# Kernel tuning notes

Measured on AMD Instinct MI355X. Metric: run time of the kernel, lower is better.

The kernel has to match this reference:

```python
import jax, jax.numpy as jnp
import numpy as np

L, H, D, HS, DFF, V, B, T = 4, 16, 1024, 64, 5120, 32000, 2, 1024
EPS = 1e-5


def setup_inputs() -> dict:
    key = jax.random.key(0)
    ks = iter(jax.random.split(key, 40))
    def nrm(shape):
        return jax.random.normal(next(ks), shape, dtype=jnp.float32) * 0.02
    inp = {}
    inp['idx'] = jax.random.randint(next(ks), (B, T), 0, V)
    inp['tok_emb'] = nrm((V, D))
    inp['pos_emb'] = nrm((T, D))
    for s in ('u', 'm'):  # u = unmasked heads, m = masked (causal) heads
        inp['Wq_' + s] = nrm((L, H, D, HS)); inp['bq_' + s] = jnp.zeros((L, H, HS), jnp.float32)
        inp['Wk_' + s] = nrm((L, H, D, HS)); inp['bk_' + s] = jnp.zeros((L, H, HS), jnp.float32)
        inp['Wv_' + s] = nrm((L, H, D, HS)); inp['bv_' + s] = jnp.zeros((L, H, HS), jnp.float32)
        inp['Wp_' + s] = nrm((L, D, D));     inp['bp_' + s] = jnp.zeros((L, D), jnp.float32)
    inp['W1'] = nrm((L, D, DFF)); inp['b1'] = jnp.zeros((L, DFF), jnp.float32)
    inp['W2'] = nrm((L, DFF, D)); inp['b2'] = jnp.zeros((L, D), jnp.float32)
    ones = jnp.ones((L, D), jnp.float32); zer = jnp.zeros((L, D), jnp.float32)
    inp['lnf_g'] = ones; inp['lnf_b'] = zer     # LayerNorm inside FeedForward
    inp['n1_g'] = ones;  inp['n1_b'] = zer      # Block.norm1
    inp['n2_g'] = ones;  inp['n2_b'] = zer      # Block.norm2
    inp['nf_g'] = jnp.ones((D,), jnp.float32); inp['nf_b'] = jnp.zeros((D,), jnp.float32)
    inp['Wfin'] = nrm((D, V)); inp['bfin'] = jnp.zeros((V,), jnp.float32)
    return inp


def _ln(x, g, b):
    mu = jnp.mean(x, -1, keepdims=True)
    var = jnp.mean((x - mu) ** 2, -1, keepdims=True)
    return (x - mu) / jnp.sqrt(var + EPS) * g + b


def _attn(xn, Wq, bq, Wk, bk, Wv, bv, Wp, bp, causal):
    # xn: [B,T,D]; Wq/Wk/Wv: [H,D,HS] (all heads batched in one einsum)
    q = jnp.einsum('btd,hde->bhte', xn, Wq) + bq[:, None, :]
    k = jnp.einsum('btd,hde->bhte', xn, Wk) + bk[:, None, :]
    v = jnp.einsum('btd,hde->bhte', xn, Wv) + bv[:, None, :]
    w = jnp.einsum('bhte,bhse->bhts', q, k) * (HS ** -0.5)
    if causal:
        mask = jnp.tril(jnp.ones((w.shape[-2], w.shape[-1]), bool))
        w = jnp.where(mask, w, -jnp.inf)
    w = jax.nn.softmax(w, axis=-1)
    o = jnp.einsum('bhts,bhse->bhte', w, v)
    o = o.transpose(0, 2, 1, 3).reshape(xn.shape[0], xn.shape[1], -1)  # concat heads
    return o @ Wp + bp


def _ffn(x, W1, b1, W2, b2, g, b):
    h = jax.nn.leaky_relu(x @ W1 + b1, negative_slope=0.01)
    return _ln(h @ W2 + b2, g, b)


def reference(idx, tok_emb, pos_emb,
              Wq_u, bq_u, Wk_u, bk_u, Wv_u, bv_u, Wp_u, bp_u,
              Wq_m, bq_m, Wk_m, bk_m, Wv_m, bv_m, Wp_m, bp_m,
              W1, b1, W2, b2, lnf_g, lnf_b, n1_g, n1_b, n2_g, n2_b,
              nf_g, nf_b, Wfin, bfin):
    Tn = idx.shape[1]
    x = tok_emb[idx] + pos_emb[:Tn]
    for l in range(L):
        # exact quirky Block wiring from the original code
        x2 = x + _attn(_ln(x, n1_g[l], n1_b[l]), Wq_u[l], bq_u[l], Wk_u[l], bk_u[l],
                       Wv_u[l], bv_u[l], Wp_u[l], bp_u[l], False)
        x = x2 + _ln(_ffn(_ln(x2, n2_g[l], n2_b[l]), W1[l], b1[l], W2[l], b2[l],
                          lnf_g[l], lnf_b[l]), n1_g[l], n1_b[l])
        x2 = x + _attn(_ln(x, n1_g[l], n1_b[l]), Wq_m[l], bq_m[l], Wk_m[l], bk_m[l],
                       Wv_m[l], bv_m[l], Wp_m[l], bp_m[l], True)
        x = x2 + _ln(_ffn(_ln(x2, n2_g[l], n2_b[l]), W1[l], b1[l], W2[l], b2[l],
                          lnf_g[l], lnf_b[l]), n2_g[l], n2_b[l])
    x = _ln(x, nf_g, nf_b)
    return x @ Wfin + bfin  # logits [B,T,V]; targets=None path -> loss is None
```

## Files before the change

kernel.cpp:

```cpp
#include <hip/hip_runtime.h>
#include <hip/hip_bf16.h>
#include <math.h>

#define LNUM 4
#define H 16
#define D 1024
#define HS 64
#define DFF 5120
#define V 32000
#define BB 2
#define T 1024
#define M (BB*T)
#define EPS 1e-5f

typedef __attribute__((ext_vector_type(8))) short bf16x8;
typedef __attribute__((ext_vector_type(4))) float f32x4;

__device__ __forceinline__ void gload16(const void* g, void* l) {
    __builtin_amdgcn_global_load_lds(
        (const __attribute__((address_space(1))) void*)g,
        (__attribute__((address_space(3))) void*)l, 16, 0, 0);
}

__device__ __forceinline__ float wred_sum(float v) {
    #pragma unroll
    for (int off = 32; off; off >>= 1) v += __shfl_xor(v, off, 64);
    return v;
}

__global__ __launch_bounds__(256) void embed_kernel(const int* __restrict__ idx,
        const float* __restrict__ tok, const float* __restrict__ pos,
        float* __restrict__ x) {
    int row = blockIdx.x;
    int t = row & (T - 1);
    int tok_id = idx[row];
    int c = threadIdx.x * 4;
    float4 a = *(const float4*)&tok[(size_t)tok_id * D + c];
    float4 p = *(const float4*)&pos[(size_t)t * D + c];
    a.x += p.x; a.y += p.y; a.z += p.z; a.w += p.w;
    *(float4*)&x[(size_t)row * D + c] = a;
}

__global__ __launch_bounds__(256) void ln_bf16_w4_kernel(const float* __restrict__ in,
        const float* __restrict__ g, const float* __restrict__ b,
        __hip_bfloat16* __restrict__ out) {
    int w = threadIdx.x >> 6, lane = threadIdx.x & 63;
    int row = blockIdx.x * 4 + w;
    const float* rp = in + (size_t)row * D;
    float4 xv[4];
    float s = 0.f;
    #pragma unroll
    for (int c = 0; c < 4; ++c) {
        xv[c] = *(const float4*)&rp[c * 256 + lane * 4];
        s += xv[c].x + xv[c].y + xv[c].z + xv[c].w;
    }
    float mu = wred_sum(s) * (1.0f / D);
    float vs = 0.f;
    #pragma unroll
    for (int c = 0; c < 4; ++c) {
        xv[c].x -= mu; xv[c].y -= mu; xv[c].z -= mu; xv[c].w -= mu;
        vs += xv[c].x*xv[c].x + xv[c].y*xv[c].y + xv[c].z*xv[c].z + xv[c].w*xv[c].w;
    }
    float rs = rsqrtf(wred_sum(vs) * (1.0f / D) + EPS);
    #pragma unroll
    for (int c = 0; c < 4; ++c) {
        int j = c * 256 + lane * 4;
        float4 gv = *(const float4*)&g[j];
        float4 bv = *(const float4*)&b[j];
        union { ushort4 u4; __hip_bfloat16 h[4]; } pk;
        pk.h[0] = __float2bfloat16(xv[c].x * rs * gv.x + bv.x);
        pk.h[1] = __float2bfloat16(xv[c].y * rs * gv.y + bv.y);
        pk.h[2] = __float2bfloat16(xv[c].z * rs * gv.z + bv.z);
        pk.h[3] = __float2bfloat16(xv[c].w * rs * gv.w + bv.w);
        *(ushort4*)&out[(size_t)row * D + j] = pk.u4;
    }
}

template<int NP>
__global__ __launch_bounds__(256) void ffn_tail_kernel(
        const float* __restrict__ part, const float* __restrict__ b2,
        const float* __restrict__ g1, const float* __restrict__ b1,
        const float* __restrict__ g2, const float* __restrict__ b2g,
        const float* __restrict__ res, float* __restrict__ xout,
        const float* __restrict__ gn, const float* __restrict__ bn,
        __hip_bfloat16* __restrict__ xnout) {
    const size_t MD = (size_t)M * D;
    int w = threadIdx.x >> 6, lane = threadIdx.x & 63;
    int row = blockIdx.x * 4 + w;
    size_t ro = (size_t)row * D;
    float4 f[4];
    float s = 0.f;
    #pragma unroll
    for (int c = 0; c < 4; ++c) {
        int j = c * 256 + lane * 4;
        float4 acc = *(const float4*)&b2[j];
        #pragma unroll
        for (int pI = 0; pI < NP; ++pI) {
            float4 pv = *(const float4*)&part[pI * MD + ro + j];
            acc.x += pv.x; acc.y += pv.y; acc.z += pv.z; acc.w += pv.w;
        }
        f[c] = acc;
        s += acc.x + acc.y + acc.z + acc.w;
    }
    float mu = wred_sum(s) * (1.0f / D);
    float vs = 0.f;
    #pragma unroll
    for (int c = 0; c < 4; ++c) {
        f[c].x -= mu; f[c].y -= mu; f[c].z -= mu; f[c].w -= mu;
        vs += f[c].x*f[c].x + f[c].y*f[c].y + f[c].z*f[c].z + f[c].w*f[c].w;
    }
    float rs = rsqrtf(wred_sum(vs) * (1.0f / D) + EPS);
    float s2 = 0.f;
    #pragma unroll
    for (int c = 0; c < 4; ++c) {
        int j = c * 256 + lane * 4;
        float4 gv = *(const float4*)&g1[j];
        float4 bv = *(const float4*)&b1[j];
        f[c].x = f[c].x * rs * gv.x + bv.x;
        f[c].y = f[c].y * rs * gv.y + bv.y;
        f[c].z = f[c].z * rs * gv.z + bv.z;
        f[c].w = f[c].w * rs * gv.w + bv.w;
        s2 += f[c].x + f[c].y + f[c].z + f[c].w;
    }
    float mu2 = wred_sum(s2) * (1.0f / D);
    float vs2 = 0.f;
    #pragma unroll
    for (int c = 0; c < 4; ++c) {
        f[c].x -= mu2; f[c].y -= mu2; f[c].z -= mu2; f[c].w -= mu2;
        vs2 += f[c].x*f[c].x + f[c].y*f[c].y + f[c].z*f[c].z + f[c].w*f[c].w;
    }
    float rs2 = rsqrtf(wred_sum(vs2) * (1.0f / D) + EPS);
    float s3 = 0.f;
    #pragma unroll
    for (int c = 0; c < 4; ++c) {
        int j = c * 256 + lane * 4;
        float4 gv = *(const float4*)&g2[j];
        float4 bv = *(const float4*)&b2g[j];
        float4 rv = *(const float4*)&res[ro + j];
        f[c].x = rv.x + f[c].x * rs2 * gv.x + bv.x;
        f[c].y = rv.y + f[c].y * rs2 * gv.y + bv.y;
        f[c].z = rv.z + f[c].z * rs2 * gv.z + bv.z;
        f[c].w = rv.w + f[c].w * rs2 * gv.w + bv.w;
        *(float4*)&xout[ro + j] = f[c];
        s3 += f[c].x + f[c].y + f[c].z + f[c].w;
    }
    float mu3 = wred_sum(s3) * (1.0f / D);
    float vs3 = 0.f;
    #pragma unroll
    for (int c = 0; c < 4; ++c) {
        f[c].x -= mu3; f[c].y -= mu3; f[c].z -= mu3; f[c].w -= mu3;
        vs3 += f[c].x*f[c].x + f[c].y*f[c].y + f[c].z*f[c].z + f[c].w*f[c].w;
    }
    float rs3 = rsqrtf(wred_sum(vs3) * (1.0f / D) + EPS);
    #pragma unroll
    for (int c = 0; c < 4; ++c) {
        int j = c * 256 + lane * 4;
        float4 gv = *(const float4*)&gn[j];
        float4 bv = *(const float4*)&bn[j];
        union { ushort4 u4; __hip_bfloat16 h[4]; } pk;
        pk.h[0] = __float2bfloat16(f[c].x * rs3 * gv.x + bv.x);
        pk.h[1] = __float2bfloat16(f[c].y * rs3 * gv.y + bv.y);
        pk.h[2] = __float2bfloat16(f[c].z * rs3 * gv.z + bv.z);
        pk.h[3] = __float2bfloat16(f[c].w * rs3 * gv.w + bv.w);
        *(ushort4*)&xnout[ro + j] = pk.u4;
    }
}

__global__ __launch_bounds__(256) void transpose_bf16_kernel(
        const float* __restrict__ in, __hip_bfloat16* __restrict__ out,
        int R, int C, size_t zin, size_t zout) {
    __shared__ float t[32][33];
    in += (size_t)blockIdx.z * zin; out += (size_t)blockIdx.z * zout;
    int tx = threadIdx.x & 31, ty = threadIdx.x >> 5;
    int c0 = blockIdx.x * 32, r0 = blockIdx.y * 32;
    #pragma unroll
    for (int i = 0; i < 4; ++i)
        t[ty + i * 8][tx] = in[(size_t)(r0 + ty + i * 8) * C + c0 + tx];
    __syncthreads();
    #pragma unroll
    for (int i = 0; i < 4; ++i)
        out[(size_t)(c0 + ty + i * 8) * R + r0 + tx] = __float2bfloat16(t[tx][ty + i * 8]);
}

__global__ __launch_bounds__(256) void transpose_qkv_kernel(
        const float* __restrict__ Wq, const float* __restrict__ Wk,
        const float* __restrict__ Wv, short* __restrict__ outT) {
    __shared__ float t[32][33];
    int z = blockIdx.z;
    int which = z >> 4, h = z & 15;
    const float* in = (which == 0 ? Wq : which == 1 ? Wk : Wv) + (size_t)h * D * HS;
    __hip_bfloat16* out = (__hip_bfloat16*)outT + ((size_t)which * H + h) * HS * D;
    int tx = threadIdx.x & 31, ty = threadIdx.x >> 5;
    int c0 = blockIdx.x * 32, r0 = blockIdx.y * 32;
    #pragma unroll
    for (int i = 0; i < 4; ++i)
        t[ty + i * 8][tx] = in[(size_t)(r0 + ty + i * 8) * HS + c0 + tx];
    __syncthreads();
    #pragma unroll
    for (int i = 0; i < 4; ++i)
        out[(size_t)(c0 + ty + i * 8) * D + r0 + tx] = __float2bfloat16(t[tx][ty + i * 8]);
}

__global__ __launch_bounds__(256) void transpose_v_kernel(const short* __restrict__ in,
        short* __restrict__ out) {
    __shared__ short t[32][33];
    int z = blockIdx.z;
    in  += (size_t)z * T * HS;
    out += (size_t)z * HS * T;
    int tx = threadIdx.x & 31, ty = threadIdx.x >> 5;
    int c0 = blockIdx.x * 32, r0 = blockIdx.y * 32;
    #pragma unroll
    for (int i = 0; i < 4; ++i)
        t[ty + i * 8][tx] = in[(size_t)(r0 + ty + i * 8) * HS + c0 + tx];
    __syncthreads();
    #pragma unroll
    for (int i = 0; i < 4; ++i)
        out[(size_t)(c0 + ty + i * 8) * T + r0 + tx] = t[tx][ty + i * 8];
}

template<int EPI>
__global__ __launch_bounds__(512, 2) void mm256_kernel(
        const short* __restrict__ A, const short* __restrict__ BT,
        const float* __restrict__ bias0, float* __restrict__ C0,
        __hip_bfloat16* __restrict__ Cbf, int N, int Kloop, int lda) {
    __shared__ __align__(16) char LA[2][2][256 * 64];
    __shared__ __align__(16) char LB[2][2][256 * 64];
    int tid = threadIdx.x;
    int lane = tid & 63, wid = tid >> 6;
    int wr = wid >> 2, wc = wid & 3;
    int l15 = lane & 15, l16 = lane >> 4;

    int nwg = gridDim.x;
    int bid = blockIdx.x;
    int q = nwg >> 3, r = nwg & 7;
    int xcd = bid & 7, loc = bid >> 3;
    int wg = (xcd < r ? xcd * (q + 1) : r * (q + 1) + (xcd - r) * q) + loc;
    int m0 = (wg & 7) * 256;
    int n0 = (wg >> 3) * 256;

    const size_t lda2 = (size_t)lda * 2;
    const char* Agc = (const char*)A + (size_t)m0 * lda2;
    const char* Bgc = (const char*)BT + (size_t)n0 * lda2;

    f32x4 acc[8][4] = {};
    bf16x8 af[8], bfr[2];

    auto stA = [&](int buf, int kh, int kt) {
        #pragma unroll
        for (int i = 0; i < 2; ++i) {
            int o = i * 8192 + tid * 16;
            int row = o >> 6, col = o & 63;
            gload16(Agc + (size_t)row * lda2 + kt * 128 + kh * 64 +
                    (col ^ (((row >> 1) & 3) << 4)), LA[buf][kh] + o);
        }
    };
    auto stB = [&](int buf, int kh, int kt) {
        #pragma unroll
        for (int i = 0; i < 2; ++i) {
            int o = i * 8192 + tid * 16;
            int row = o >> 6, col = o & 63;
            gload16(Bgc + (size_t)row * lda2 + kt * 128 + kh * 64 +
                    (col ^ (((row >> 1) & 3) << 4)), LB[buf][kh] + o);
        }
    };
    auto rdA = [&](int buf, int kk) {
        #pragma unroll
        for (int mf = 0; mf < 8; ++mf) {
            int row = wr * 128 + mf * 16 + l15;
            af[mf] = *(const bf16x8*)(LA[buf][kk] + row * 64 +
                      ((l16 * 16) ^ (((row >> 1) & 3) << 4)));
        }
    };
    auto rdB = [&](int buf, int kk, int nh) {
        #pragma unroll
        for (int nf = 0; nf < 2; ++nf) {
            int row = wc * 64 + nh * 32 + nf * 16 + l15;
            bfr[nf] = *(const bf16x8*)(LB[buf][kk] + row * 64 +
                       ((l16 * 16) ^ (((row >> 1) & 3) << 4)));
        }
    };
    auto mfma16 = [&](int nh) {
        __builtin_amdgcn_s_setprio(1);
        #pragma unroll
        for (int mf = 0; mf < 8; ++mf) {
            acc[mf][nh * 2 + 0] = __builtin_amdgcn_mfma_f32_16x16x32_bf16(
                af[mf], bfr[0], acc[mf][nh * 2 + 0], 0, 0, 0);
            acc[mf][nh * 2 + 1] = __builtin_amdgcn_mfma_f32_16x16x32_bf16(
                af[mf], bfr[1], acc[mf][nh * 2 + 1], 0, 0, 0);
        }
        __builtin_amdgcn_s_setprio(0);
        __builtin_amdgcn_s_barrier();
    };

    const int NT = Kloop / 64;
    stA(0, 0, 0); stB(0, 0, 0); stA(0, 1, 0); stB(0, 1, 0);
    stA(1, 0, 1); stB(1, 0, 1);

    for (int t = 0; t < NT; ++t) {
        int buf = t & 1;
        if (t + 1 < NT) { asm volatile("s_waitcnt vmcnt(4)" ::: "memory"); }
        else            { asm volatile("s_waitcnt vmcnt(0)" ::: "memory"); }
        __builtin_amdgcn_sched_barrier(0);
        __builtin_amdgcn_s_barrier();
        __builtin_amdgcn_sched_barrier(0);
        rdA(buf, 0); rdB(buf, 0, 0);
        if (t + 1 < NT) stA(buf ^ 1, 1, t + 1);
        __builtin_amdgcn_s_barrier();
        asm volatile("s_waitcnt lgkmcnt(0)" ::: "memory");
        __builtin_amdgcn_sched_barrier(0);
        mfma16(0);
        rdB(buf, 0, 1);
        if (t + 1 < NT) stB(buf ^ 1, 1, t + 1);
        __builtin_amdgcn_s_barrier();
        asm volatile("s_waitcnt lgkmcnt(0)" ::: "memory");
        __builtin_amdgcn_sched_barrier(0);
        mfma16(1);
        rdA(buf, 1); rdB(buf, 1, 0);
        if (t + 2 < NT) stA(buf, 0, t + 2);
        __builtin_amdgcn_s_barrier();
        asm volatile("s_waitcnt lgkmcnt(0)" ::: "memory");
        __builtin_amdgcn_sched_barrier(0);
        mfma16(0);
        rdB(buf, 1, 1);
        if (t + 2 < NT) stB(buf, 0, t + 2);
        __builtin_amdgcn_s_barrier();
        asm volatile("s_waitcnt lgkmcnt(0)" ::: "memory");
        __builtin_amdgcn_sched_barrier(0);
        mfma16(1);
    }

    #pragma unroll
    for (int mf = 0; mf < 8; ++mf) {
        #pragma unroll
        for (int nf = 0; nf < 4; ++nf) {
            int col = n0 + wc * 64 + nf * 16 + l15;
            float bv = bias0[col];
            #pragma unroll
            for (int rr = 0; rr < 4; ++rr) {
                int row = m0 + wr * 128 + mf * 16 + l16 * 4 + rr;
                float v = acc[mf][nf][rr] + bv;
                if (EPI == 0) {
                    C0[(size_t)row * N + col] = v;
                } else {
                    v = v > 0.f ? v : 0.01f * v;
                    Cbf[(size_t)row * N + col] = __float2bfloat16(v);
                }
            }
        }
    }
}

template<int BM, int EPI>
__global__ __launch_bounds__(256) void mm_bf16_kernel(
        const short* __restrict__ A, const short* __restrict__ BT,
        const float* __restrict__ bias0, const float* __restrict__ bias1,
        const float* __restrict__ bias2, const float* __restrict__ res,
        float* __restrict__ C0, float* __restrict__ C1, float* __restrict__ C2,
        __hip_bfloat16* __restrict__ Cbf, int N, int Kloop, int lda) {
    constexpr int MI = BM / 32;
    __shared__ __align__(16) char As[2][BM * 128];
    __shared__ __align__(16) char Bs[2][128 * 128];
    int nwg = gridDim.x * gridDim.y;
    int bid = blockIdx.y * gridDim.x + blockIdx.x;
    int bx = blockIdx.x, by = blockIdx.y;
    if (!(nwg & 7)) {
        int s = (bid & 7) * (nwg >> 3) + (bid >> 3);
        bx = s % gridDim.x; by = s / gridDim.x;
    }
    int tid = threadIdx.x;
    int lane = tid & 63, wid = tid >> 6;
    int wr = wid >> 1, wc = wid & 1;
    int l15 = lane & 15, l16 = lane >> 4;
    int m0 = bx * BM, n0 = by * 128;
    f32x4 acc[MI][4] = {};

    const size_t lda2 = (size_t)lda * 2;
    const char* Agc = (const char*)A + (size_t)m0 * lda2 + (size_t)blockIdx.z * Kloop * 2;
    const char* Bgc = (const char*)BT + (size_t)n0 * lda2 + (size_t)blockIdx.z * Kloop * 2;

    auto stage = [&](int buf, int kbyte) {
        #pragma unroll
        for (int i = 0; i < BM / 32; ++i) {
            int o = i * 4096 + tid * 16;
            int row = o >> 7, col = o & 127;
            gload16(Agc + (size_t)row * lda2 + kbyte + (col ^ ((row & 7) << 4)),
                    As[buf] + o);
        }
        #pragma unroll
        for (int i = 0; i < 4; ++i) {
            int o = i * 4096 + tid * 16;
            int row = o >> 7, col = o & 127;
            gload16(Bgc + (size_t)row * lda2 + kbyte + (col ^ ((row & 7) << 4)),
                    Bs[buf] + o);
        }
    };
    auto compute = [&](int buf) {
        #pragma unroll
        for (int kk = 0; kk < 2; ++kk) {
            bf16x8 af[MI], bfr[4];
            #pragma unroll
            for (int mi = 0; mi < MI; ++mi) {
                int row = wr * (BM / 2) + mi * 16 + l15;
                af[mi] = *(const bf16x8*)(As[buf] + row * 128 +
                          ((kk * 64 + l16 * 16) ^ ((row & 7) << 4)));
            }
            #pragma unroll
            for (int ni = 0; ni < 4; ++ni) {
                int row = wc * 64 + ni * 16 + l15;
                bfr[ni] = *(const bf16x8*)(Bs[buf] + row * 128 +
                          ((kk * 64 + l16 * 16) ^ ((row & 7) << 4)));
            }
            __builtin_amdgcn_s_setprio(1);
            #pragma unroll
            for (int mi = 0; mi < MI; ++mi)
                #pragma unroll
                for (int ni = 0; ni < 4; ++ni)
                    acc[mi][ni] = __builtin_amdgcn_mfma_f32_16x16x32_bf16(
                        af[mi], bfr[ni], acc[mi][ni], 0, 0, 0);
            __builtin_amdgcn_s_setprio(0);
        }
    };

    const int NT = Kloop / 64;
    stage(0, 0);
    stage(1, 128);
    for (int t = 0; t < NT; ++t) {
        if (t < NT - 1) {
            if constexpr (BM == 128) asm volatile("s_waitcnt vmcnt(8)" ::: "memory");
            else                     asm volatile("s_waitcnt vmcnt(6)" ::: "memory");
        } else {
            asm volatile("s_waitcnt vmcnt(0)" ::: "memory");
        }
        __builtin_amdgcn_sched_barrier(0);
        __builtin_amdgcn_s_barrier();
        __builtin_amdgcn_sched_barrier(0);
        compute(t & 1);
        __builtin_amdgcn_s_barrier();
        __builtin_amdgcn_sched_barrier(0);
        if (t + 2 < NT) stage(t & 1, (t + 2) * 128);
    }

    int rbase = m0 + wr * (BM / 2) + l16 * 4;
    int cbase = n0 + wc * 64 + l15;
    size_t zoff = (EPI == 4) ? (size_t)blockIdx.z * M * N : 0;
    #pragma unroll
    for (int mi = 0; mi < MI; ++mi) {
        #pragma unroll
        for (int ni = 0; ni < 4; ++ni) {
            int col = cbase + ni * 16;
            float bv = 0.f;
            if (EPI == 3) {
                int z = col >> 10, nn = col & 1023;
                bv = (z == 0 ? bias0 : z == 1 ? bias1 : bias2)[nn];
            } else if (EPI != 4) bv = bias0[col];
            #pragma unroll
            for (int r = 0; r < 4; ++r) {
                int row = rbase + mi * 16 + r;
                float v = acc[mi][ni][r] + bv;
                if (EPI == 0) {
                    C0[(size_t)row * N + col] = v;
                } else if (EPI == 1) {
                    C0[(size_t)row * N + col] = v + res[(size_t)row * N + col];
                } else if (EPI == 2) {
                    v = v > 0.f ? v : 0.01f * v;
                    Cbf[(size_t)row * N + col] = __float2bfloat16(v);
                } else if (EPI == 4) {
                    C0[zoff + (size_t)row * N + col] = v;
                } else {
                    int z = col >> 10;
                    int hh = (col >> 6) & 15, e = col & 63;
                    int b = row >> 10, t2 = row & (T - 1);
                    __hip_bfloat16* dst = (__hip_bfloat16*)(z == 0 ? C0 : (z == 1 ? C1 : C2));
                    dst[(((size_t)(b * H + hh)) * T + t2) * HS + e] = __float2bfloat16(v);
                }
            }
        }
    }
}

template<int CAUSAL>
__global__ __launch_bounds__(256) void attn_mfma_kernel(
        const short* __restrict__ q, const short* __restrict__ k,
        const short* __restrict__ vt, __hip_bfloat16* __restrict__ att) {
    __shared__ __align__(16) short Ks[128 * 64];
    __shared__ __align__(16) short Vs[64 * 128];
    __shared__ __align__(16) short Ps[4][16 * 128];
    int bh = blockIdx.y;
    int bI = bh >> 4, h = bh & 15;
    int tix = blockIdx.x;
    if (CAUSAL) tix = (tix & 1) ? (15 - (tix >> 1)) : (tix >> 1);
    int t0 = tix * 64;
    int tid = threadIdx.x;
    int lane = tid & 63, w = tid >> 6;
    int l15 = lane & 15, l16 = lane >> 4;

    const short* Qg = q + ((size_t)bh * T + t0 + w * 16 + l15) * HS + l16 * 8;
    bf16x8 qf0 = *(const bf16x8*)Qg;
    bf16x8 qf1 = *(const bf16x8*)(Qg + 32);

    const char* Kg = (const char*)(k + (size_t)bh * T * HS);
    const char* Vg = (const char*)(vt + (size_t)bh * HS * T);

    float m_run[4] = {-1e30f, -1e30f, -1e30f, -1e30f};
    float l_run[4] = {0.f, 0.f, 0.f, 0.f};
    f32x4 acc_o[4] = {};
    char* Pw = (char*)Ps[w];
    int pswz = l15 << 4;

    int n_tiles = CAUSAL ? (t0 / 128 + 1) : (T / 128);
    for (int it = 0; it < n_tiles; ++it) {
        int s0 = it * 128;
        __syncthreads();
        #pragma unroll
        for (int i = 0; i < 4; ++i) {
            int o = i * 4096 + tid * 16;
            int row = o >> 7, bir = o & 127;
            gload16(Kg + (size_t)(s0 + row) * 128 + (bir ^ ((row & 7) << 4)),
                    (char*)Ks + o);
        }
        #pragma unroll
        for (int i = 0; i < 4; ++i) {
            int o = i * 4096 + tid * 16;
            int row = o >> 8, bb = o & 255;
            gload16(Vg + (size_t)row * 2048 + s0 * 2 + (bb ^ ((row & 15) << 4)),
                    (char*)Vs + o);
        }
        __syncthreads();

        f32x4 acc_s[8] = {};
        __builtin_amdgcn_s_setprio(1);
        #pragma unroll
        for (int c = 0; c < 8; ++c) {
            int row = c * 16 + l15;
            const char* kb_ = (const char*)Ks + row * 128;
            int swz = (row & 7) << 4;
            bf16x8 kf0 = *(const bf16x8*)(kb_ + ((l16 * 16) ^ swz));
            bf16x8 kf1 = *(const bf16x8*)(kb_ + ((64 + l16 * 16) ^ swz));
            acc_s[c] = __builtin_amdgcn_mfma_f32_16x16x32_bf16(qf0, kf0, acc_s[c], 0, 0, 0);
            acc_s[c] = __builtin_amdgcn_mfma_f32_16x16x32_bf16(qf1, kf1, acc_s[c], 0, 0, 0);
        }
        __builtin_amdgcn_s_setprio(0);

        bool domask = CAUSAL && (it == n_tiles - 1);
        #pragma unroll
        for (int r = 0; r < 4; ++r) {
            float sc[8];
            #pragma unroll
            for (int c = 0; c < 8; ++c) {
                float s = acc_s[c][r];
                if (domask && (s0 + c * 16 + l15) > (t0 + w * 16 + l16 * 4 + r)) s = -1e30f;
                sc[c] = s;
            }
            float tm = fmaxf(fmaxf(fmaxf(sc[0], sc[1]), fmaxf(sc[2], sc[3])),
                             fmaxf(fmaxf(sc[4], sc[5]), fmaxf(sc[6], sc[7])));
            tm = fmaxf(tm, __shfl_xor(tm, 1, 16));
            tm = fmaxf(tm, __shfl_xor(tm, 2, 16));
            tm = fmaxf(tm, __shfl_xor(tm, 4, 16));
            tm = fmaxf(tm, __shfl_xor(tm, 8, 16));
            float mn = fmaxf(m_run[r], tm);
            int prow = l16 * 4 + r;
            int pswzr = prow << 4;
            float ls = 0.f;
            #pragma unroll
            for (int c = 0; c < 8; ++c) {
                float pv = __expf(0.125f * (sc[c] - mn));
                int pbyte = prow * 256 + (((c * 16 + l15) * 2) ^ pswzr);
                *(__hip_bfloat16*)(Pw + pbyte) = __float2bfloat16(pv);
                ls += pv;
            }
            ls += __shfl_xor(ls, 1, 16);
            ls += __shfl_xor(ls, 2, 16);
            ls += __shfl_xor(ls, 4, 16);
            ls += __shfl_xor(ls, 8, 16);
            float alpha = __expf(0.125f * (m_run[r] - mn));
            l_run[r] = l_run[r] * alpha + ls;
            m_run[r] = mn;
            acc_o[0][r] *= alpha; acc_o[1][r] *= alpha;
            acc_o[2][r] *= alpha; acc_o[3][r] *= alpha;
        }

        const char* Pb = Pw + l15 * 256;
        bf16x8 pa[4];
        #pragma unroll
        for (int t = 0; t < 4; ++t)
            pa[t] = *(const bf16x8*)(Pb + ((t * 64 + l16 * 16) ^ pswz));
        __builtin_amdgcn_s_setprio(1);
        #pragma unroll
        for (int ni = 0; ni < 4; ++ni) {
            int row = ni * 16 + l15;
            const char* vb_ = (const char*)Vs + row * 256;
            int swz = (row & 15) << 4;
            #pragma unroll
            for (int t = 0; t < 4; ++t) {
                bf16x8 vf = *(const bf16x8*)(vb_ + ((t * 64 + l16 * 16) ^ swz));
                acc_o[ni] = __builtin_amdgcn_mfma_f32_16x16x32_bf16(pa[t], vf, acc_o[ni], 0, 0, 0);
            }
        }
        __builtin_amdgcn_s_setprio(0);
    }

    float inv[4];
    #pragma unroll
    for (int r = 0; r < 4; ++r) inv[r] = 1.0f / l_run[r];
    #pragma unroll
    for (int ni = 0; ni < 4; ++ni) {
        #pragma unroll
        for (int r = 0; r < 4; ++r) {
            size_t orow = ((size_t)(bI * T) + t0 + w * 16 + l16 * 4 + r) * D
                        + h * HS + ni * 16 + l15;
            att[orow] = __float2bfloat16(acc_o[ni][r] * inv[r]);
        }
    }
}

extern "C" void kernel_launch(void* const* d_in, const int* in_sizes, int n_in,
                              void* d_out, int out_size, void* d_ws, size_t ws_size,
                              hipStream_t stream) {
    const int*   idx     = (const int*)d_in[0];
    const float* tok_emb = (const float*)d_in[1];
    const float* pos_emb = (const float*)d_in[2];
    const float* Wq_u = (const float*)d_in[3],  *bq_u = (const float*)d_in[4];
    const float* Wk_u = (const float*)d_in[5],  *bk_u = (const float*)d_in[6];
    const float* Wv_u = (const float*)d_in[7],  *bv_u = (const float*)d_in[8];
    const float* Wp_u = (const float*)d_in[9],  *bp_u = (const float*)d_in[10];
    const float* Wq_m = (const float*)d_in[11], *bq_m = (const float*)d_in[12];
    const float* Wk_m = (const float*)d_in[13], *bk_m = (const float*)d_in[14];
    const float* Wv_m = (const float*)d_in[15], *bv_m = (const float*)d_in[16];
    const float* Wp_m = (const float*)d_in[17], *bp_m = (const float*)d_in[18];
    const float* W1   = (const float*)d_in[19], *b1   = (const float*)d_in[20];
    const float* W2   = (const float*)d_in[21], *b2   = (const float*)d_in[22];
    const float* lnf_g = (const float*)d_in[23], *lnf_b = (const float*)d_in[24];
    const float* n1_g  = (const float*)d_in[25], *n1_b  = (const float*)d_in[26];
    const float* n2_g  = (const float*)d_in[27], *n2_b  = (const float*)d_in[28];
    const float* nf_g  = (const float*)d_in[29], *nf_b  = (const float*)d_in[30];
    const float* Wfin  = (const float*)d_in[31], *bfin  = (const float*)d_in[32];
    float* out = (float*)d_out;

    char* p = (char*)d_ws;
    auto alloc = [&](size_t bytes) { char* r = p; p += (bytes + 255) & ~255ull; return r; };
    float* x    = (float*)alloc((size_t)M * D * 4);
    float* x2   = (float*)alloc((size_t)M * D * 4);
    float* w2p  = (float*)alloc((size_t)4 * M * D * 4);
    short* qbf  = (short*)alloc((size_t)M * D * 2);
    short* kbf  = (short*)alloc((size_t)M * D * 2);
    short* vbf  = (short*)alloc((size_t)M * D * 2);
    short* vtb  = (short*)alloc((size_t)M * D * 2);
    short* xnb  = (short*)alloc((size_t)M * D * 2);
    short* attb = (short*)alloc((size_t)M * D * 2);
    short* hb   = (short*)alloc((size_t)M * DFF * 2);
    short* WqkvT= (short*)alloc((size_t)3 * 1024 * 1024 * 2);
    short* WpT  = (short*)alloc((size_t)1024 * 1024 * 2);
    short* W1T  = (short*)alloc((size_t)D * DFF * 2);
    short* W2T  = (short*)alloc((size_t)DFF * D * 2);
    short* WfT  = (short*)alloc((size_t)D * V * 2);

    embed_kernel<<<M, 256, 0, stream>>>(idx, tok_emb, pos_emb, x);
    ln_bf16_w4_kernel<<<M / 4, 256, 0, stream>>>(x, n1_g, n1_b, (__hip_bfloat16*)xnb);
    transpose_bf16_kernel<<<dim3(V / 32, D / 32, 1), 256, 0, stream>>>(
        Wfin, (__hip_bfloat16*)WfT, D, V, 0, 0);

    for (int l = 0; l < LNUM; ++l) {
        const float *n1g = n1_g + l * D, *n1b = n1_b + l * D;
        const float *n2g = n2_g + l * D, *n2b = n2_b + l * D;
        const float *lfg = lnf_g + l * D, *lfb = lnf_b + l * D;
        const float *W1l = W1 + (size_t)l * D * DFF, *b1l = b1 + l * DFF;
        const float *W2l = W2 + (size_t)l * DFF * D, *b2l = b2 + l * D;
        transpose_bf16_kernel<<<dim3(DFF / 32, D / 32, 1), 256, 0, stream>>>(
            W1l, (__hip_bfloat16*)W1T, D, DFF, 0, 0);
        transpose_bf16_kernel<<<dim3(D / 32, DFF / 32, 1), 256, 0, stream>>>(
            W2l, (__hip_bfloat16*)W2T, DFF, D, 0, 0);
        for (int half = 0; half < 2; ++half) {
            const float *Wq_, *bq_, *Wk_, *bk_, *Wv_, *bv_, *Wp_, *bp_;
            if (half == 0) { Wq_ = Wq_u; bq_ = bq_u; Wk_ = Wk_u; bk_ = bk_u;
                             Wv_ = Wv_u; bv_ = bv_u; Wp_ = Wp_u; bp_ = bp_u; }
            else           { Wq_ = Wq_m; bq_ = bq_m; Wk_ = Wk_m; bk_ = bk_m;
                             Wv_ = Wv_m; bv_ = bv_m; Wp_ = Wp_m; bp_ = bp_m; }
            Wq_ += (size_t)l * H * D * HS;  bq_ += l * H * HS;
            Wk_ += (size_t)l * H * D * HS;  bk_ += l * H * HS;
            Wv_ += (size_t)l * H * D * HS;  bv_ += l * H * HS;
            Wp_ += (size_t)l * D * D;       bp_ += l * D;

            transpose_qkv_kernel<<<dim3(HS / 32, D / 32, 48), 256, 0, stream>>>(
                Wq_, Wk_, Wv_, WqkvT);
            transpose_bf16_kernel<<<dim3(D / 32, D / 32, 1), 256, 0, stream>>>(
                Wp_, (__hip_bfloat16*)WpT, D, D, 0, 0);

            mm_bf16_kernel<128, 3><<<dim3(M / 128, 3072 / 128), 256, 0, stream>>>(
                xnb, WqkvT, bq_, bk_, bv_, nullptr,
                (float*)qbf, (float*)kbf, (float*)vbf, nullptr, 3072, D, D);
            transpose_v_kernel<<<dim3(HS / 32, T / 32, BB * H), 256, 0, stream>>>(vbf, vtb);
            if (half == 0)
                attn_mfma_kernel<0><<<dim3(T / 64, BB * H), 256, 0, stream>>>(
                    qbf, kbf, vtb, (__hip_bfloat16*)attb);
            else
                attn_mfma_kernel<1><<<dim3(T / 64, BB * H), 256, 0, stream>>>(
                    qbf, kbf, vtb, (__hip_bfloat16*)attb);
            mm_bf16_kernel<64, 1><<<dim3(M / 64, D / 128), 256, 0, stream>>>(
                attb, WpT, bp_, nullptr, nullptr, x, x2, nullptr, nullptr, nullptr, D, D, D);
            ln_bf16_w4_kernel<<<M / 4, 256, 0, stream>>>(x2, n2g, n2b, (__hip_bfloat16*)xnb);
            mm256_kernel<2><<<(M / 256) * (DFF / 256), 512, 0, stream>>>(
                xnb, W1T, b1l, nullptr, (__hip_bfloat16*)hb, DFF, D, D);
            mm_bf16_kernel<128, 4><<<dim3(M / 128, D / 128, 4), 256, 0, stream>>>(
                hb, W2T, nullptr, nullptr, nullptr, nullptr, w2p, nullptr, nullptr,
                nullptr, D, DFF / 4, DFF);
            const float* og = half ? n2g : n1g;
            const float* ob = half ? n2b : n1b;
            const float* gn; const float* bn;
            if (half == 0)      { gn = n1g; bn = n1b; }
            else if (l < LNUM-1){ gn = n1_g + (l+1)*D; bn = n1_b + (l+1)*D; }
            else                { gn = nf_g; bn = nf_b; }
            ffn_tail_kernel<4><<<M / 4, 256, 0, stream>>>(
                w2p, b2l, lfg, lfb, og, ob, x2, x, gn, bn, (__hip_bfloat16*)xnb);
        }
    }
    mm256_kernel<0><<<(M / 256) * (V / 256), 512, 0, stream>>>(
        xnb, WfT, bfin, out, nullptr, V, D, D);
}
```

Before: 1.589 ms.

## Fuse embedding with LayerNorm, merge weight transposes, simplify mm256 pipeline

Folds the embedding add and the first LayerNorm into one kernel and merges the per-layer weight transpose launches (W1+W2, Wq/Wk/Wv+Wp) into single launches. This removes several kernel launches and one full pass over the activations. It also restructures the mm256 main loop to load all four B fragments at once and issue 32 MFMAs per half-step, with fewer barriers and no explicit LDS waits. That cuts synchronisation, but it raises register pressure and may expose more LDS latency.

```diff
diff --git a/kernel.cpp b/kernel.cpp
--- a/kernel.cpp
+++ b/kernel.cpp
@@ -28,17 +28,48 @@
     return v;
 }
 
-__global__ __launch_bounds__(256) void embed_kernel(const int* __restrict__ idx,
+__global__ __launch_bounds__(256) void embed_ln_kernel(const int* __restrict__ idx,
         const float* __restrict__ tok, const float* __restrict__ pos,
-        float* __restrict__ x) {
-    int row = blockIdx.x;
+        const float* __restrict__ g, const float* __restrict__ b,
+        float* __restrict__ x, __hip_bfloat16* __restrict__ xn) {
+    int w = threadIdx.x >> 6, lane = threadIdx.x & 63;
+    int row = blockIdx.x * 4 + w;
     int t = row & (T - 1);
     int tok_id = idx[row];
-    int c = threadIdx.x * 4;
-    float4 a = *(const float4*)&tok[(size_t)tok_id * D + c];
-    float4 p = *(const float4*)&pos[(size_t)t * D + c];
-    a.x += p.x; a.y += p.y; a.z += p.z; a.w += p.w;
-    *(float4*)&x[(size_t)row * D + c] = a;
+    const float* tp = tok + (size_t)tok_id * D;
+    const float* pp = pos + (size_t)t * D;
+    float4 xv[4];
+    float s = 0.f;
+    #pragma unroll
+    for (int c = 0; c < 4; ++c) {
+        int j = c * 256 + lane * 4;
+        float4 a = *(const float4*)&tp[j];
+        float4 p = *(const float4*)&pp[j];
+        a.x += p.x; a.y += p.y; a.z += p.z; a.w += p.w;
+        *(float4*)&x[(size_t)row * D + j] = a;
+        xv[c] = a;
+        s += a.x + a.y + a.z + a.w;
+    }
+    float mu = wred_sum(s) * (1.0f / D);
+    float vs = 0.f;
+    #pragma unroll
+    for (int c = 0; c < 4; ++c) {
+        xv[c].x -= mu; xv[c].y -= mu; xv[c].z -= mu; xv[c].w -= mu;
+        vs += xv[c].x*xv[c].x + xv[c].y*xv[c].y + xv[c].z*xv[c].z + xv[c].w*xv[c].w;
+    }
+    float rs = rsqrtf(wred_sum(vs) * (1.0f / D) + EPS);
+    #pragma unroll
+    for (int c = 0; c < 4; ++c) {
+        int j = c * 256 + lane * 4;
+        float4 gv = *(const float4*)&g[j];
+        float4 bv = *(const float4*)&b[j];
+        union { ushort4 u4; __hip_bfloat16 h[4]; } pk;
+        pk.h[0] = __float2bfloat16(xv[c].x * rs * gv.x + bv.x);
+        pk.h[1] = __float2bfloat16(xv[c].y * rs * gv.y + bv.y);
+        pk.h[2] = __float2bfloat16(xv[c].z * rs * gv.z + bv.z);
+        pk.h[3] = __float2bfloat16(xv[c].w * rs * gv.w + bv.w);
+        *(ushort4*)&xn[(size_t)row * D + j] = pk.u4;
+    }
 }
 
 __global__ __launch_bounds__(256) void ln_bf16_w4_kernel(const float* __restrict__ in,
@@ -168,9 +199,8 @@
 
 __global__ __launch_bounds__(256) void transpose_bf16_kernel(
         const float* __restrict__ in, __hip_bfloat16* __restrict__ out,
-        int R, int C, size_t zin, size_t zout) {
+        int R, int C) {
     __shared__ float t[32][33];
-    in += (size_t)blockIdx.z * zin; out += (size_t)blockIdx.z * zout;
     int tx = threadIdx.x & 31, ty = threadIdx.x >> 5;
     int c0 = blockIdx.x * 32, r0 = blockIdx.y * 32;
     #pragma unroll
@@ -182,23 +212,57 @@
         out[(size_t)(c0 + ty + i * 8) * R + r0 + tx] = __float2bfloat16(t[tx][ty + i * 8]);
 }
 
-__global__ __launch_bounds__(256) void transpose_qkv_kernel(
+__global__ __launch_bounds__(256) void trans_qkvp_kernel(
         const float* __restrict__ Wq, const float* __restrict__ Wk,
-        const float* __restrict__ Wv, short* __restrict__ outT) {
+        const float* __restrict__ Wv, const float* __restrict__ Wp,
+        short* __restrict__ qkvT, short* __restrict__ WpT) {
     __shared__ float t[32][33];
+    int tx = threadIdx.x & 31, ty = threadIdx.x >> 5;
     int z = blockIdx.z;
-    int which = z >> 4, h = z & 15;
-    const float* in = (which == 0 ? Wq : which == 1 ? Wk : Wv) + (size_t)h * D * HS;
-    __hip_bfloat16* out = (__hip_bfloat16*)outT + ((size_t)which * H + h) * HS * D;
+    const float* in;
+    __hip_bfloat16* out;
+    int inC, outC;
+    int r0 = blockIdx.y * 32, c0;
+    if (z < 3) {
+        int c0g = blockIdx.x * 32;
+        int h = c0g >> 6;
+        c0 = c0g & 63;
+        in = (z == 0 ? Wq : z == 1 ? Wk : Wv) + (size_t)h * D * HS;
+        out = (__hip_bfloat16*)qkvT + ((size_t)z * H + h) * HS * D;
+        inC = HS; outC = D;
+    } else {
+        c0 = blockIdx.x * 32;
+        in = Wp; out = (__hip_bfloat16*)WpT;
+        inC = D; outC = D;
+    }
+    #pragma unroll
+    for (int i = 0; i < 4; ++i)
+        t[ty + i * 8][tx] = in[(size_t)(r0 + ty + i * 8) * inC + c0 + tx];
+    __syncthreads();
+    #pragma unroll
+    for (int i = 0; i < 4; ++i)
+        out[(size_t)(c0 + ty + i * 8) * outC + r0 + tx] = __float2bfloat16(t[tx][ty + i * 8]);
+}
+
+__global__ __launch_bounds__(256) void trans_w12_kernel(
+        const float* __restrict__ W1, const float* __restrict__ W2,
+        short* __restrict__ W1T, short* __restrict__ W2T) {
+    __shared__ float t[32][33];
     int tx = threadIdx.x & 31, ty = threadIdx.x >> 5;
-    int c0 = blockIdx.x * 32, r0 = blockIdx.y * 32;
+    int z = blockIdx.z;
+    const float* in; __hip_bfloat16* out;
+    int inC, outC, r0, c0;
+    if (z == 0) { in = W1; out = (__hip_bfloat16*)W1T; inC = DFF; outC = D;
+                  r0 = blockIdx.y * 32; c0 = blockIdx.x * 32; }
+    else        { in = W2; out = (__hip_bfloat16*)W2T; inC = D; outC = DFF;
+                  r0 = blockIdx.x * 32; c0 = blockIdx.y * 32; }
     #pragma unroll
     for (int i = 0; i < 4; ++i)
-        t[ty + i * 8][tx] = in[(size_t)(r0 + ty + i * 8) * HS + c0 + tx];
+        t[ty + i * 8][tx] = in[(size_t)(r0 + ty + i * 8) * inC + c0 + tx];
     __syncthreads();
     #pragma unroll
     for (int i = 0; i < 4; ++i)
-        out[(size_t)(c0 + ty + i * 8) * D + r0 + tx] = __float2bfloat16(t[tx][ty + i * 8]);
+        out[(size_t)(c0 + ty + i * 8) * outC + r0 + tx] = __float2bfloat16(t[tx][ty + i * 8]);
 }
 
 __global__ __launch_bounds__(256) void transpose_v_kernel(const short* __restrict__ in,
@@ -243,7 +307,7 @@
     const char* Bgc = (const char*)BT + (size_t)n0 * lda2;
 
     f32x4 acc[8][4] = {};
-    bf16x8 af[8], bfr[2];
+    bf16x8 af[8], bfr[4];
 
     auto stA = [&](int buf, int kh, int kt) {
         #pragma unroll
@@ -271,62 +335,49 @@
                       ((l16 * 16) ^ (((row >> 1) & 3) << 4)));
         }
     };
-    auto rdB = [&](int buf, int kk, int nh) {
-        #pragma unroll
-        for (int nf = 0; nf < 2; ++nf) {
-            int row = wc * 64 + nh * 32 + nf * 16 + l15;
+    auto rdB4 = [&](int buf, int kk) {
+        #pragma unroll
+        for (int nf = 0; nf < 4; ++nf) {
+            int row = wc * 64 + nf * 16 + l15;
             bfr[nf] = *(const bf16x8*)(LB[buf][kk] + row * 64 +
                        ((l16 * 16) ^ (((row >> 1) & 3) << 4)));
         }
     };
-    auto mfma16 = [&](int nh) {
+    auto mfma32 = [&]() {
         __builtin_amdgcn_s_setprio(1);
         #pragma unroll
-        for (int mf = 0; mf < 8; ++mf) {
-            acc[mf][nh * 2 + 0] = __builtin_amdgcn_mfma_f32_16x16x32_bf16(
-                af[mf], bfr[0], acc[mf][nh * 2 + 0], 0, 0, 0);
-            acc[mf][nh * 2 + 1] = __builtin_amdgcn_mfma_f32_16x16x32_bf16(
-                af[mf], bfr[1], acc[mf][nh * 2 + 1], 0, 0, 0);
-        }
+        for (int mf = 0; mf < 8; ++mf)
+            #pragma unroll
+            for (int nf = 0; nf < 4; ++nf)
+                acc[mf][nf] = __builtin_amdgcn_mfma_f32_16x16x32_bf16(
+                    af[mf], bfr[nf], acc[mf][nf], 0, 0, 0);
         __builtin_amdgcn_s_setprio(0);
-        __builtin_amdgcn_s_barrier();
     };
 
     const int NT = Kloop / 64;
     stA(0, 0, 0); stB(0, 0, 0); stA(0, 1, 0); stB(0, 1, 0);
     stA(1, 0, 1); stB(1, 0, 1);
+    asm volatile("s_waitcnt vmcnt(4)" ::: "memory");
+    __builtin_amdgcn_sched_barrier(0);
+    __builtin_amdgcn_s_barrier();
+    __builtin_amdgcn_sched_barrier(0);
 
     for (int t = 0; t < NT; ++t) {
         int buf = t & 1;
-        if (t + 1 < NT) { asm volatile("s_waitcnt vmcnt(4)" ::: "memory"); }
+        rdA(buf, 0); rdB4(buf, 0);
+        if (t + 1 < NT) { stA(buf ^ 1, 1, t + 1); stB(buf ^ 1, 1, t + 1); }
+        mfma32();
+        __builtin_amdgcn_sched_barrier(0);
+        __builtin_amdgcn_s_barrier();
+        __builtin_amdgcn_sched_barrier(0);
+        rdA(buf, 1); rdB4(buf, 1);
+        if (t + 2 < NT) { stA(buf, 0, t + 2); stB(buf, 0, t + 2); }
+        mfma32();
+        if (t + 2 < NT) { asm volatile("s_waitcnt vmcnt(4)" ::: "memory"); }
         else            { asm volatile("s_waitcnt vmcnt(0)" ::: "memory"); }
         __builtin_amdgcn_sched_barrier(0);
         __builtin_amdgcn_s_barrier();
         __builtin_amdgcn_sched_barrier(0);
-        rdA(buf, 0); rdB(buf, 0, 0);
-        if (t + 1 < NT) stA(buf ^ 1, 1, t + 1);
-        __builtin_amdgcn_s_barrier();
-        asm volatile("s_waitcnt lgkmcnt(0)" ::: "memory");
-        __builtin_amdgcn_sched_barrier(0);
-        mfma16(0);
-        rdB(buf, 0, 1);
-        if (t + 1 < NT) stB(buf ^ 1, 1, t + 1);
-        __builtin_amdgcn_s_barrier();
-        asm volatile("s_waitcnt lgkmcnt(0)" ::: "memory");
-        __builtin_amdgcn_sched_barrier(0);
-        mfma16(1);
-        rdA(buf, 1); rdB(buf, 1, 0);
-        if (t + 2 < NT) stA(buf, 0, t + 2);
-        __builtin_amdgcn_s_barrier();
-        asm volatile("s_waitcnt lgkmcnt(0)" ::: "memory");
-        __builtin_amdgcn_sched_barrier(0);
-        mfma16(0);
-        rdB(buf, 1, 1);
-        if (t + 2 < NT) stB(buf, 0, t + 2);
-        __builtin_amdgcn_s_barrier();
-        asm volatile("s_waitcnt lgkmcnt(0)" ::: "memory");
-        __builtin_amdgcn_sched_barrier(0);
-        mfma16(1);
     }
 
     #pragma unroll
@@ -654,10 +705,10 @@
     short* W2T  = (short*)alloc((size_t)DFF * D * 2);
     short* WfT  = (short*)alloc((size_t)D * V * 2);
 
-    embed_kernel<<<M, 256, 0, stream>>>(idx, tok_emb, pos_emb, x);
-    ln_bf16_w4_kernel<<<M / 4, 256, 0, stream>>>(x, n1_g, n1_b, (__hip_bfloat16*)xnb);
-    transpose_bf16_kernel<<<dim3(V / 32, D / 32, 1), 256, 0, stream>>>(
-        Wfin, (__hip_bfloat16*)WfT, D, V, 0, 0);
+    embed_ln_kernel<<<M / 4, 256, 0, stream>>>(idx, tok_emb, pos_emb,
+        n1_g, n1_b, x, (__hip_bfloat16*)xnb);
+    transpose_bf16_kernel<<<dim3(V / 32, D / 32), 256, 0, stream>>>(
+        Wfin, (__hip_bfloat16*)WfT, D, V);
 
     for (int l = 0; l < LNUM; ++l) {
         const float *n1g = n1_g + l * D, *n1b = n1_b + l * D;
@@ -665,10 +716,8 @@
         const float *lfg = lnf_g + l * D, *lfb = lnf_b + l * D;
         const float *W1l = W1 + (size_t)l * D * DFF, *b1l = b1 + l * DFF;
         const float *W2l = W2 + (size_t)l * DFF * D, *b2l = b2 + l * D;
-        transpose_bf16_kernel<<<dim3(DFF / 32, D / 32, 1), 256, 0, stream>>>(
-            W1l, (__hip_bfloat16*)W1T, D, DFF, 0, 0);
-        transpose_bf16_kernel<<<dim3(D / 32, DFF / 32, 1), 256, 0, stream>>>(
-            W2l, (__hip_bfloat16*)W2T, DFF, D, 0, 0);
+        trans_w12_kernel<<<dim3(160, 32, 2), 256, 0, stream>>>(
+            W1l, W2l, W1T, W2T);
         for (int half = 0; half < 2; ++half) {
             const float *Wq_, *bq_, *Wk_, *bk_, *Wv_, *bv_, *Wp_, *bp_;
             if (half == 0) { Wq_ = Wq_u; bq_ = bq_u; Wk_ = Wk_u; bk_ = bk_u;
@@ -680,10 +729,8 @@
             Wv_ += (size_t)l * H * D * HS;  bv_ += l * H * HS;
             Wp_ += (size_t)l * D * D;       bp_ += l * D;
 
-            transpose_qkv_kernel<<<dim3(HS / 32, D / 32, 48), 256, 0, stream>>>(
-                Wq_, Wk_, Wv_, WqkvT);
-            transpose_bf16_kernel<<<dim3(D / 32, D / 32, 1), 256, 0, stream>>>(
-                Wp_, (__hip_bfloat16*)WpT, D, D, 0, 0);
+            trans_qkvp_kernel<<<dim3(32, 32, 4), 256, 0, stream>>>(
+                Wq_, Wk_, Wv_, Wp_, WqkvT, WpT);
 
             mm_bf16_kernel<128, 3><<<dim3(M / 128, 3072 / 128), 256, 0, stream>>>(
                 xnb, WqkvT, bq_, bk_, bv_, nullptr,
```

Result: faster. 1.519 ms (-4.4%).
